# Kernel tuning notes

Hardware: AMD Instinct MI355X
Metric: run time of the kernel (lower is better)

## Reference

```python
import jax, jax.numpy as jnp
import numpy as np

B, S, D, H, L, MLP, WIN = 4, 1024, 256, 8, 2, 1024, 64
HD = D // H
NEG = -1e9  # emulates -inf additive mask; exp underflows to exact 0

_idx = jnp.arange(S)
BAND = jnp.where(jnp.abs(_idx[:, None] - _idx[None, :]) <= WIN, 0.0, NEG).astype(jnp.float32)


def setup_inputs() -> dict:
    key = jax.random.key(0)
    ks = iter(jax.random.split(key, 16))
    r = lambda shape, s=0.02: jax.random.normal(next(ks), shape, dtype=jnp.float32) * s
    return {
        "x": jax.random.normal(next(ks), (B, S, D), dtype=jnp.float32),
        "scale": jnp.ones((1,), jnp.float32) * (D ** -0.5),
        "Win_a": r((L, 3 * D, D)), "bin_a": jnp.zeros((L, 3 * D), jnp.float32),
        "Wout_a": r((L, D, D)), "bout_a": jnp.zeros((L, D), jnp.float32),
        "Win_e": r((L, 3 * D, D)), "bin_e": jnp.zeros((L, 3 * D), jnp.float32),
        "Wout_e": r((L, D, D)), "bout_e": jnp.zeros((L, D), jnp.float32),
        "ln1_g": jnp.ones((L, D), jnp.float32), "ln1_b": jnp.zeros((L, D), jnp.float32),
        "ln2_g": jnp.ones((L, D), jnp.float32), "ln2_b": jnp.zeros((L, D), jnp.float32),
        "W1": r((L, MLP, D)), "b1": jnp.zeros((L, MLP), jnp.float32),
        "W2": r((L, D, MLP)), "b2": jnp.zeros((L, D), jnp.float32),
        "lnf_g": jnp.ones((D,), jnp.float32), "lnf_b": jnp.zeros((D,), jnp.float32),
    }


def _layernorm(x, g, b, eps=1e-5):
    m = jnp.mean(x, axis=-1, keepdims=True)
    v = jnp.mean(jnp.square(x - m), axis=-1, keepdims=True)
    return (x - m) * jax.lax.rsqrt(v + eps) * g + b


def _mha(x, Win, bin_, Wout, bout, mask=None):
    # torch nn.MultiheadAttention (batch_first=True), dropout=0
    b, s, _ = x.shape
    qkv = x @ Win.T + bin_                       # (b, s, 3D)
    q, k, v = jnp.split(qkv, 3, axis=-1)
    split = lambda t: t.reshape(b, s, H, HD).transpose(0, 2, 1, 3)  # (b, H, s, HD)
    q, k, v = split(q), split(k), split(v)
    scores = jnp.einsum('bhqd,bhkd->bhqk', q, k) / np.float32(np.sqrt(HD))
    if mask is not None:
        scores = scores + mask
    attn = jax.nn.softmax(scores, axis=-1)
    out = jnp.einsum('bhqk,bhkd->bhqd', attn, v).transpose(0, 2, 1, 3).reshape(b, s, D)
    return out @ Wout.T + bout


def reference(x, scale, Win_a, bin_a, Wout_a, bout_a, Win_e, bin_e, Wout_e, bout_e,
              ln1_g, ln1_b, ln2_g, ln2_b, W1, b1, W2, b2, lnf_g, lnf_b):
    # ScaledSinusoidalPositionalEncoding returns arange(S)*scale, shape (S,1)
    pos = jnp.arange(S, dtype=jnp.float32) * scale[0]   # (S,)
    x = x + pos[:, None]                                 # broadcast (B,S,D)+(S,1)
    for l in range(L):
        xi = _mha(x, Win_a[l], bin_a[l], Wout_a[l], bout_a[l])
        x = _layernorm(x + xi, ln1_g[l], ln1_b[l])
        xe = _mha(x, Win_e[l], bin_e[l], Wout_e[l], bout_e[l], mask=BAND)
        attended = _layernorm(x + xe, ln2_g[l], ln2_b[l])
        h = jax.nn.gelu(attended @ W1[l].T + b1[l], approximate=False)
        x = attended + h @ W2[l].T + b2[l]
    return _layernorm(x, lnf_g, lnf_b)
```

## Files before the change

### kernel.cpp

```cpp
#include <hip/hip_runtime.h>
#include <math.h>

#define BB 4
#define SS 1024
#define DD 256
#define HH 8
#define HD 32
#define D3 768
#define MLP 1024
#define NTOK (BB * SS)
#define NSEG 4

typedef __attribute__((ext_vector_type(8))) short short8;
typedef __attribute__((ext_vector_type(4))) float f32x4;

__device__ __forceinline__ unsigned short f2bfu(float f) {
    union { float f; unsigned i; } u; u.f = f;
    unsigned r = u.i + 0x7fffu + ((u.i >> 16) & 1u);
    return (unsigned short)(r >> 16);
}
__device__ __forceinline__ float bfu2f(unsigned short h) {
    union { unsigned i; float f; } u; u.i = ((unsigned)h) << 16; return u.f;
}

#define W_TOT 2097152
#define WL0   196608
#define WBLK  (W_TOT / 256)
#define PBLK  (NTOK * DD / 256)
__global__ __launch_bounds__(256) void prep_kernel(
    const float* __restrict__ a0, const float* __restrict__ a1,
    const float* __restrict__ a2, const float* __restrict__ a3,
    const float* __restrict__ a4, const float* __restrict__ a5,
    unsigned short* __restrict__ out, unsigned short* __restrict__ out_lo,
    const float* __restrict__ x, const float* __restrict__ scale,
    float* __restrict__ xf, unsigned short* __restrict__ xh,
    unsigned short* __restrict__ xl)
{
    if (blockIdx.x < WBLK) {
        int i = blockIdx.x * 256 + threadIdx.x;
        const float* s; int off;
        if      (i <  393216) { s = a0; off = 0;       }
        else if (i <  524288) { s = a1; off = 393216;  }
        else if (i <  917504) { s = a2; off = 524288;  }
        else if (i < 1048576) { s = a3; off = 917504;  }
        else if (i < 1572864) { s = a4; off = 1048576; }
        else                  { s = a5; off = 1572864; }
        float v = s[i - off];
        unsigned short h = f2bfu(v);
        out[i] = h;
        if (i < WL0) out_lo[i] = f2bfu(v - bfu2f(h));
    } else {
        int i = (blockIdx.x - WBLK) * 256 + threadIdx.x;
        int s = (i >> 8) & (SS - 1);
        float v = x[i] + (float)s * scale[0];
        xf[i] = v;
        unsigned short h = f2bfu(v);
        xh[i] = h;
        xl[i] = f2bfu(v - bfu2f(h));
    }
}

__device__ __forceinline__ size_t vt_index(int row, int col512) {
    int b = row >> 10, s = row & (SS - 1);
    int h = col512 >> 5, d = col512 & (HD - 1);
    return (((size_t)b * HH + h) * HD + d) * SS + s;
}

#define LDP 40
__global__ __launch_bounds__(256) void gemm_mfma(
    const unsigned short* __restrict__ A, const unsigned short* __restrict__ W,
    const float* __restrict__ bias, const float* __restrict__ resid,
    float* __restrict__ outf, unsigned short* __restrict__ outb,
    unsigned short* __restrict__ vth,
    int M, int N, int K, int act)
{
    __shared__ __align__(16) unsigned short As[64 * LDP];
    __shared__ __align__(16) unsigned short Bs[128 * LDP];
    const int t = threadIdx.x;
    const int lane = t & 63, wave = t >> 6;
    const int wr = wave >> 1, wc = wave & 1;
    const int m0 = blockIdx.y * 64, n0 = blockIdx.x * 128;
    const int sr = t >> 2;
    const int sc = (t & 3) * 8;

    const unsigned short* Ag = A + (size_t)(m0 + sr) * K + sc;
    const unsigned short* Wg = W + (size_t)(n0 + sr) * K + sc;

    f32x4 acc[2][4];
    #pragma unroll
    for (int i = 0; i < 2; i++)
        #pragma unroll
        for (int j = 0; j < 4; j++)
            acc[i][j] = (f32x4){0.f, 0.f, 0.f, 0.f};

    const int lm = lane & 15, lk = (lane >> 4) * 8;

    uint4 a0 = *(const uint4*)(Ag);
    uint4 b0 = *(const uint4*)(Wg);
    uint4 b1 = *(const uint4*)(Wg + (size_t)64 * K);

    for (int k0 = 0; k0 < K; k0 += 32) {
        __syncthreads();
        *(uint4*)&As[sr * LDP + sc]        = a0;
        *(uint4*)&Bs[sr * LDP + sc]        = b0;
        *(uint4*)&Bs[(sr + 64) * LDP + sc] = b1;
        __syncthreads();
        if (k0 + 32 < K) {
            a0 = *(const uint4*)(Ag + k0 + 32);
            b0 = *(const uint4*)(Wg + k0 + 32);
            b1 = *(const uint4*)(Wg + (size_t)64 * K + k0 + 32);
        }

        short8 af[2], bf[4];
        #pragma unroll
        for (int i = 0; i < 2; i++)
            af[i] = *(const short8*)&As[(wr * 32 + i * 16 + lm) * LDP + lk];
        #pragma unroll
        for (int j = 0; j < 4; j++)
            bf[j] = *(const short8*)&Bs[(wc * 64 + j * 16 + lm) * LDP + lk];
        #pragma unroll
        for (int i = 0; i < 2; i++)
            #pragma unroll
            for (int j = 0; j < 4; j++)
                acc[i][j] = __builtin_amdgcn_mfma_f32_16x16x32_bf16(
                    af[i], bf[j], acc[i][j], 0, 0, 0);
    }

    const int lq = lane >> 4;
    #pragma unroll
    for (int j = 0; j < 4; j++) {
        int col = n0 + wc * 64 + j * 16 + lm;
        float bv = bias[col];
        #pragma unroll
        for (int i = 0; i < 2; i++) {
            #pragma unroll
            for (int r = 0; r < 4; r++) {
                int row = m0 + wr * 32 + i * 16 + lq * 4 + r;
                float v = acc[i][j][r] + bv;
                if (act) v = 0.5f * v * (1.0f + erff(v * 0.70710678118654752f));
                if (vth && col >= 2 * DD) {
                    vth[vt_index(row, col - 2 * DD)] = f2bfu(v);
                } else {
                    size_t idx = (size_t)row * N + col;
                    if (resid) v += resid[idx];
                    if (outf) outf[idx] = v;
                    if (outb) outb[idx] = f2bfu(v);
                }
            }
        }
    }
}

template<bool COMBINE, bool DOLN, int K>
__global__ __launch_bounds__(256) void gemm_ln(
    const unsigned short* __restrict__ A,
    const float* __restrict__ Of, const float2* __restrict__ Ml,
    const unsigned short* __restrict__ W, const float* __restrict__ bias,
    const float* __restrict__ resid,
    const float* __restrict__ g, const float* __restrict__ bt,
    float* __restrict__ outf, unsigned short* __restrict__ outb)
{
    constexpr int LDA = K + 8;
    constexpr int NS  = K / 32;
    __shared__ __align__(16) unsigned short As[16 * LDA];
    __shared__ float rsum[4][16];
    __shared__ float rsum2[4][16];
    const int t = threadIdx.x;
    const int lane = t & 63, wave = t >> 6;
    const int m0 = blockIdx.x * 16;
    const int lm = lane & 15, quad = lane >> 4;

    const unsigned short* Wp = W + (size_t)(wave * 64 + lm) * K + quad * 8;
    short8 bf[4][4];
    #pragma unroll
    for (int s = 0; s < 4; s++)
        #pragma unroll
        for (int j = 0; j < 4; j++)
            bf[s][j] = *(const short8*)(Wp + (size_t)(j * 16) * K + s * 32);

    if (COMBINE) {
        const int row = t >> 4, cg = t & 15;
        const int token = m0 + row;
        const int h = cg >> 1;
        float2 ml[NSEG];
        float M = -1e30f;
        #pragma unroll
        for (int s = 0; s < NSEG; s++) {
            ml[s] = Ml[((size_t)s * NTOK + token) * HH + h];
            M = fmaxf(M, ml[s].x);
        }
        float wgt[NSEG]; float denom = 0.f;
        #pragma unroll
        for (int s = 0; s < NSEG; s++) {
            wgt[s] = __expf(ml[s].x - M);
            denom += ml[s].y * wgt[s];
        }
        const float inv = 1.0f / denom;
        float a16[16];
        #pragma unroll
        for (int c = 0; c < 16; c++) a16[c] = 0.f;
        #pragma unroll
        for (int s = 0; s < NSEG; s++) {
            const float* p = Of + ((size_t)s * NTOK + token) * DD + cg * 16;
            #pragma unroll
            for (int c4 = 0; c4 < 4; c4++) {
                float4 x = *(const float4*)(p + c4 * 4);
                a16[c4 * 4 + 0] += x.x * wgt[s];
                a16[c4 * 4 + 1] += x.y * wgt[s];
                a16[c4 * 4 + 2] += x.z * wgt[s];
                a16[c4 * 4 + 3] += x.w * wgt[s];
            }
        }
        __align__(16) unsigned short ab[16];
        #pragma unroll
        for (int c = 0; c < 16; c++) ab[c] = f2bfu(a16[c] * inv);
        *(uint4*)&As[row * LDA + cg * 16]     = *(uint4*)&ab[0];
        *(uint4*)&As[row * LDA + cg * 16 + 8] = *(uint4*)&ab[8];
    } else {
        #pragma unroll
        for (int u = t; u < 16 * (K / 8); u += 256) {
            int row = u / (K / 8), cg = u % (K / 8);
            *(uint4*)&As[row * LDA + cg * 8] =
                *(const uint4*)(A + (size_t)(m0 + row) * K + cg * 8);
        }
    }
    __syncthreads();

    f32x4 acc[4];
    #pragma unroll
    for (int j = 0; j < 4; j++) acc[j] = (f32x4){0.f, 0.f, 0.f, 0.f};

    #pragma unroll
    for (int k = 0; k < NS; k++) {
        const int r4 = k & 3;
        short8 af = *(const short8*)&As[lm * LDA + k * 32 + quad * 8];
        #pragma unroll
        for (int j = 0; j < 4; j++)
            acc[j] = __builtin_amdgcn_mfma_f32_16x16x32_bf16(
                af, bf[r4][j], acc[j], 0, 0, 0);
        if (k + 4 < NS) {
            #pragma unroll
            for (int j = 0; j < 4; j++)
                bf[r4][j] = *(const short8*)(Wp + (size_t)(j * 16) * K
                                             + (k + 4) * 32);
        }
    }

    #pragma unroll
    for (int j = 0; j < 4; j++) {
        int col = wave * 64 + j * 16 + lm;
        float bv = bias[col];
        #pragma unroll
        for (int r = 0; r < 4; r++) {
            int row = m0 + quad * 4 + r;
            acc[j][r] += bv + resid[(size_t)row * DD + col];
        }
    }
    if (!DOLN) {
        #pragma unroll
        for (int j = 0; j < 4; j++) {
            int col = wave * 64 + j * 16 + lm;
            #pragma unroll
            for (int r = 0; r < 4; r++) {
                int row = m0 + quad * 4 + r;
                size_t idx = (size_t)row * DD + col;
                if (outf) outf[idx] = acc[j][r];
                if (outb) outb[idx] = f2bfu(acc[j][r]);
            }
        }
        return;
    }
    #pragma unroll
    for (int r = 0; r < 4; r++) {
        float s = 0.f;
        #pragma unroll
        for (int j = 0; j < 4; j++) s += acc[j][r];
        s += __shfl_xor(s, 1, 64); s += __shfl_xor(s, 2, 64);
        s += __shfl_xor(s, 4, 64); s += __shfl_xor(s, 8, 64);
        if (lm == 0) rsum[wave][quad * 4 + r] = s;
    }
    __syncthreads();
    float mean_[4];
    #pragma unroll
    for (int r = 0; r < 4; r++) {
        int ri = quad * 4 + r;
        mean_[r] = (rsum[0][ri] + rsum[1][ri] + rsum[2][ri] + rsum[3][ri])
                 * (1.0f / 256.0f);
    }
    #pragma unroll
    for (int r = 0; r < 4; r++) {
        float s2 = 0.f;
        #pragma unroll
        for (int j = 0; j < 4; j++) {
            float d = acc[j][r] - mean_[r];
            s2 += d * d;
        }
        s2 += __shfl_xor(s2, 1, 64); s2 += __shfl_xor(s2, 2, 64);
        s2 += __shfl_xor(s2, 4, 64); s2 += __shfl_xor(s2, 8, 64);
        if (lm == 0) rsum2[wave][quad * 4 + r] = s2;
    }
    __syncthreads();
    float rstd[4];
    #pragma unroll
    for (int r = 0; r < 4; r++) {
        int ri = quad * 4 + r;
        rstd[r] = rsqrtf((rsum2[0][ri] + rsum2[1][ri] + rsum2[2][ri] + rsum2[3][ri])
                         * (1.0f / 256.0f) + 1e-5f);
    }
    #pragma unroll
    for (int j = 0; j < 4; j++) {
        int col = wave * 64 + j * 16 + lm;
        float gv = g[col], bv2 = bt[col];
        #pragma unroll
        for (int r = 0; r < 4; r++) {
            int row = m0 + quad * 4 + r;
            float ov = (acc[j][r] - mean_[r]) * rstd[r] * gv + bv2;
            size_t idx = (size_t)row * DD + col;
            if (outf) outf[idx] = ov;
            if (outb) outb[idx] = f2bfu(ov);
        }
    }
}

__global__ __launch_bounds__(256) void gemm_mfma_split(
    const unsigned short* __restrict__ Ah, const unsigned short* __restrict__ Al,
    const unsigned short* __restrict__ Wh, const unsigned short* __restrict__ Wl,
    const float* __restrict__ bias,
    unsigned short* __restrict__ outh, unsigned short* __restrict__ outl,
    unsigned short* __restrict__ vth,
    int M, int N, int K)
{
    __shared__ __align__(16) unsigned short Ash[64 * LDP];
    __shared__ __align__(16) unsigned short Asl[64 * LDP];
    __shared__ __align__(16) unsigned short Bsh[128 * LDP];
    __shared__ __align__(16) unsigned short Bsl[128 * LDP];
    const int t = threadIdx.x;
    const int lane = t & 63, wave = t >> 6;
    const int wr = wave >> 1, wc = wave & 1;
    const int m0 = blockIdx.y * 64, n0 = blockIdx.x * 128;
    const int sr = t >> 2;
    const int sc = (t & 3) * 8;

    const size_t oA = (size_t)(m0 + sr) * K + sc;
    const size_t oW = (size_t)(n0 + sr) * K + sc;

    f32x4 acc[2][4];
    #pragma unroll
    for (int i = 0; i < 2; i++)
        #pragma unroll
        for (int j = 0; j < 4; j++)
            acc[i][j] = (f32x4){0.f, 0.f, 0.f, 0.f};

    const int lm = lane & 15, lk = (lane >> 4) * 8;

    uint4 ah0 = *(const uint4*)(Ah + oA);
    uint4 al0 = *(const uint4*)(Al + oA);
    uint4 bh0 = *(const uint4*)(Wh + oW);
    uint4 bh1 = *(const uint4*)(Wh + oW + (size_t)64 * K);
    uint4 bl0 = *(const uint4*)(Wl + oW);
    uint4 bl1 = *(const uint4*)(Wl + oW + (size_t)64 * K);

    for (int k0 = 0; k0 < K; k0 += 32) {
        __syncthreads();
        *(uint4*)&Ash[sr * LDP + sc]        = ah0;
        *(uint4*)&Asl[sr * LDP + sc]        = al0;
        *(uint4*)&Bsh[sr * LDP + sc]        = bh0;
        *(uint4*)&Bsh[(sr + 64) * LDP + sc] = bh1;
        *(uint4*)&Bsl[sr * LDP + sc]        = bl0;
        *(uint4*)&Bsl[(sr + 64) * LDP + sc] = bl1;
        __syncthreads();
        if (k0 + 32 < K) {
            ah0 = *(const uint4*)(Ah + oA + k0 + 32);
            al0 = *(const uint4*)(Al + oA + k0 + 32);
            bh0 = *(const uint4*)(Wh + oW + k0 + 32);
            bh1 = *(const uint4*)(Wh + oW + (size_t)64 * K + k0 + 32);
            bl0 = *(const uint4*)(Wl + oW + k0 + 32);
            bl1 = *(const uint4*)(Wl + oW + (size_t)64 * K + k0 + 32);
        }

        short8 afh[2], afl[2], bfh[4], bfl[4];
        #pragma unroll
        for (int i = 0; i < 2; i++) {
            afh[i] = *(const short8*)&Ash[(wr * 32 + i * 16 + lm) * LDP + lk];
            afl[i] = *(const short8*)&Asl[(wr * 32 + i * 16 + lm) * LDP + lk];
        }
        #pragma unroll
        for (int j = 0; j < 4; j++) {
            bfh[j] = *(const short8*)&Bsh[(wc * 64 + j * 16 + lm) * LDP + lk];
            bfl[j] = *(const short8*)&Bsl[(wc * 64 + j * 16 + lm) * LDP + lk];
        }
        #pragma unroll
        for (int i = 0; i < 2; i++)
            #pragma unroll
            for (int j = 0; j < 4; j++) {
                acc[i][j] = __builtin_amdgcn_mfma_f32_16x16x32_bf16(
                    afl[i], bfh[j], acc[i][j], 0, 0, 0);
                acc[i][j] = __builtin_amdgcn_mfma_f32_16x16x32_bf16(
                    afh[i], bfl[j], acc[i][j], 0, 0, 0);
                acc[i][j] = __builtin_amdgcn_mfma_f32_16x16x32_bf16(
                    afh[i], bfh[j], acc[i][j], 0, 0, 0);
            }
    }

    const int lq = lane >> 4;
    #pragma unroll
    for (int j = 0; j < 4; j++) {
        int col = n0 + wc * 64 + j * 16 + lm;
        float bv = bias[col];
        #pragma unroll
        for (int i = 0; i < 2; i++) {
            #pragma unroll
            for (int r = 0; r < 4; r++) {
                int row = m0 + wr * 32 + i * 16 + lq * 4 + r;
                float v = acc[i][j][r] + bv;
                unsigned short h = f2bfu(v);
                if (col >= 2 * DD) {
                    vth[vt_index(row, col - 2 * DD)] = h;
                } else {
                    size_t idx = (size_t)row * N + col;
                    outh[idx] = h;
                    outl[idx] = f2bfu(v - bfu2f(h));
                }
            }
        }
    }
}

__global__ __launch_bounds__(256) void attn_split(
    const unsigned short* __restrict__ qkvh,
    const unsigned short* __restrict__ qkvl,
    const unsigned short* __restrict__ vth,
    float* __restrict__ Of, float2* __restrict__ Ml)
{
    __shared__ __align__(16) unsigned short Ks [64 * 40];
    __shared__ __align__(16) unsigned short Vt [32 * 72];
    __shared__ __align__(16) unsigned short Ps [64 * 72];
    __shared__ __align__(16) unsigned short Ksl[64 * 40];

    const int t = threadIdx.x;
    const int wave = t >> 6, lane = t & 63;
    const int lm = lane & 15, quad = lane >> 4;
    const int i0 = blockIdx.x * 64, h = blockIdx.y;
    const int z = blockIdx.z;
    const int b = z >> 2, seg = z & (NSEG - 1);
    const int sr = t >> 2, sc8 = (t & 3) * 8;
    const int vd = t >> 3, vs8 = (t & 7) * 8;

    const size_t qoff = ((size_t)(b * SS) + i0 + 16 * wave + lm) * D3 + h * HD + quad * 8;
    short8 qh = *(const short8*)(qkvh + qoff);
    short8 ql = *(const short8*)(qkvl + qoff);

    const unsigned short* Kg  = qkvh + (size_t)(b * SS) * D3 + DD + h * HD;
    const unsigned short* Klg = qkvl + (size_t)(b * SS) * D3 + DD + h * HD;
    const unsigned short* Vg  = vth + ((size_t)b * HH + h) * HD * SS;

    float m[4], l[4];
    f32x4 o[2];
    #pragma unroll
    for (int r = 0; r < 4; r++) { m[r] = -1e30f; l[r] = 0.f; }
    o[0] = (f32x4){0.f, 0.f, 0.f, 0.f};
    o[1] = (f32x4){0.f, 0.f, 0.f, 0.f};

    const int per = (SS / 64) / NSEG;
    const int s0 = seg * per, s1 = s0 + per - 1;
    const float scl = 0.17677669529663688f;

    short8 kreg  = *(const short8*)(Kg  + (size_t)(s0 * 64 + sr) * D3 + sc8);
    short8 kregl = *(const short8*)(Klg + (size_t)(s0 * 64 + sr) * D3 + sc8);
    short8 vreg  = *(const short8*)(Vg  + (size_t)vd * SS + s0 * 64 + vs8);

    for (int kt = s0; kt <= s1; kt++) {
        const int k0 = kt * 64;
        __syncthreads();
        *(short8*)&Ks [sr * 40 + sc8] = kreg;
        *(short8*)&Ksl[sr * 40 + sc8] = kregl;
        *(short8*)&Vt [vd * 72 + vs8] = vreg;
        __syncthreads();
        if (kt < s1) {
            kreg  = *(const short8*)(Kg  + (size_t)(k0 + 64 + sr) * D3 + sc8);
            kregl = *(const short8*)(Klg + (size_t)(k0 + 64 + sr) * D3 + sc8);
            vreg  = *(const short8*)(Vg  + (size_t)vd * SS + k0 + 64 + vs8);
        }

        f32x4 s[4];
        #pragma unroll
        for (int cb = 0; cb < 4; cb++) {
            short8 kf  = *(const short8*)&Ks [(16 * cb + lm) * 40 + quad * 8];
            short8 kfl = *(const short8*)&Ksl[(16 * cb + lm) * 40 + quad * 8];
            f32x4 a = (f32x4){0.f, 0.f, 0.f, 0.f};
            a = __builtin_amdgcn_mfma_f32_16x16x32_bf16(ql, kf,  a, 0, 0, 0);
            a = __builtin_amdgcn_mfma_f32_16x16x32_bf16(qh, kfl, a, 0, 0, 0);
            a = __builtin_amdgcn_mfma_f32_16x16x32_bf16(qh, kf,  a, 0, 0, 0);
            s[cb] = a;
        }

        #pragma unroll
        for (int r = 0; r < 4; r++) {
            float s0r = s[0][r] * scl, s1r = s[1][r] * scl;
            float s2r = s[2][r] * scl, s3r = s[3][r] * scl;
            float tm = fmaxf(fmaxf(s0r, s1r), fmaxf(s2r, s3r));
            tm = fmaxf(tm, __shfl_xor(tm, 1, 64));
            tm = fmaxf(tm, __shfl_xor(tm, 2, 64));
            tm = fmaxf(tm, __shfl_xor(tm, 4, 64));
            tm = fmaxf(tm, __shfl_xor(tm, 8, 64));
            float mn = fmaxf(m[r], tm);
            float alpha = __expf(m[r] - mn);
            float p0 = __expf(s0r - mn), p1 = __expf(s1r - mn);
            float p2 = __expf(s2r - mn), p3 = __expf(s3r - mn);
            float ps = p0 + p1 + p2 + p3;
            ps += __shfl_xor(ps, 1, 64);
            ps += __shfl_xor(ps, 2, 64);
            ps += __shfl_xor(ps, 4, 64);
            ps += __shfl_xor(ps, 8, 64);
            l[r] = l[r] * alpha + ps;
            o[0][r] *= alpha;
            o[1][r] *= alpha;
            m[r] = mn;
            const int pr = (16 * wave + quad * 4 + r) * 72 + lm;
            Ps[pr +  0] = f2bfu(p0);
            Ps[pr + 16] = f2bfu(p1);
            Ps[pr + 32] = f2bfu(p2);
            Ps[pr + 48] = f2bfu(p3);
        }

        #pragma unroll
        for (int kc = 0; kc < 2; kc++) {
            short8 pf = *(const short8*)&Ps[(16 * wave + lm) * 72 + 32 * kc + quad * 8];
            #pragma unroll
            for (int nh = 0; nh < 2; nh++) {
                short8 vf = *(const short8*)&Vt[(16 * nh + lm) * 72 + 32 * kc + quad * 8];
                o[nh] = __builtin_amdgcn_mfma_f32_16x16x32_bf16(pf, vf, o[nh], 0, 0, 0);
            }
        }
    }

    #pragma unroll
    for (int r = 0; r < 4; r++) {
        int row = i0 + 16 * wave + quad * 4 + r;
        size_t base = ((size_t)seg * NTOK + b * SS + row) * DD + h * HD + lm;
        Of[base]      = o[0][r];
        Of[base + 16] = o[1][r];
        if (lm == 0)
            Ml[((size_t)seg * NTOK + b * SS + row) * HH + h] =
                make_float2(m[r], l[r]);
    }
}

__global__ __launch_bounds__(256) void attn_fixed(
    const unsigned short* __restrict__ qkvh,
    const unsigned short* __restrict__ vth,
    unsigned short* __restrict__ outb,
    float* __restrict__ Of, float2* __restrict__ Ml,
    int win, int nseg)
{
    __shared__ __align__(16) unsigned short Ks[64 * 40];
    __shared__ __align__(16) unsigned short Vt[32 * 72];
    __shared__ __align__(16) unsigned short Ps[64 * 72];

    const int t = threadIdx.x;
    const int wave = t >> 6, lane = t & 63;
    const int lm = lane & 15, quad = lane >> 4;
    const int i0 = blockIdx.x * 64, h = blockIdx.y;
    const int z = blockIdx.z;
    const int b = z / nseg, seg = z - b * nseg;
    const int sr = t >> 2, sc8 = (t & 3) * 8;
    const int vd = t >> 3, vs8 = (t & 7) * 8;

    const size_t qoff = ((size_t)(b * SS) + i0 + 16 * wave + lm) * D3 + h * HD + quad * 8;
    short8 qh = *(const short8*)(qkvh + qoff);

    const unsigned short* Kg = qkvh + (size_t)(b * SS) * D3 + DD + h * HD;
    const unsigned short* Vg = vth + ((size_t)b * HH + h) * HD * SS;

    float l[4] = {0.f, 0.f, 0.f, 0.f};
    f32x4 o[2];
    o[0] = (f32x4){0.f, 0.f, 0.f, 0.f};
    o[1] = (f32x4){0.f, 0.f, 0.f, 0.f};

    int t0 = 0, t1 = SS / 64 - 1;
    const bool masked = (win < SS);
    if (masked) {
        t0 = (i0 - win) >> 6;        if (t0 < 0) t0 = 0;
        t1 = (i0 + 63 + win) >> 6;   if (t1 > SS / 64 - 1) t1 = SS / 64 - 1;
    }
    const int per = (t1 - t0 + nseg) / nseg;
    const int s0 = t0 + seg * per;
    const int s1 = (s0 + per - 1 < t1) ? (s0 + per - 1) : t1;
    const float scl = 0.17677669529663688f;
    const float M0 = 32.0f;

    short8 kreg = *(const short8*)(Kg + (size_t)(s0 * 64 + sr) * D3 + sc8);
    short8 vreg = *(const short8*)(Vg + (size_t)vd * SS + s0 * 64 + vs8);

    for (int kt = s0; kt <= s1; kt++) {
        const int k0 = kt * 64;
        __syncthreads();
        *(short8*)&Ks[sr * 40 + sc8] = kreg;
        *(short8*)&Vt[vd * 72 + vs8] = vreg;
        __syncthreads();
        if (kt < s1) {
            kreg = *(const short8*)(Kg + (size_t)(k0 + 64 + sr) * D3 + sc8);
            vreg = *(const short8*)(Vg + (size_t)vd * SS + k0 + 64 + vs8);
        }

        f32x4 s[4];
        #pragma unroll
        for (int cb = 0; cb < 4; cb++) {
            short8 kf = *(const short8*)&Ks[(16 * cb + lm) * 40 + quad * 8];
            f32x4 a = (f32x4){0.f, 0.f, 0.f, 0.f};
            a = __builtin_amdgcn_mfma_f32_16x16x32_bf16(qh, kf, a, 0, 0, 0);
            s[cb] = a;
        }

        #pragma unroll
        for (int r = 0; r < 4; r++) {
            float p[4];
            #pragma unroll
            for (int cb = 0; cb < 4; cb++) {
                float v = s[cb][r] * scl;
                if (masked) {
                    int di = (i0 + 16 * wave + quad * 4 + r) - (k0 + 16 * cb + lm);
                    if (di > win || di < -win) v = -1e30f;
                }
                p[cb] = __expf(v - M0);
            }
            l[r] += p[0] + p[1] + p[2] + p[3];
            const int pr = (16 * wave + quad * 4 + r) * 72 + lm;
            Ps[pr +  0] = f2bfu(p[0]);
            Ps[pr + 16] = f2bfu(p[1]);
            Ps[pr + 32] = f2bfu(p[2]);
            Ps[pr + 48] = f2bfu(p[3]);
        }

        #pragma unroll
        for (int kc = 0; kc < 2; kc++) {
            short8 pf = *(const short8*)&Ps[(16 * wave + lm) * 72 + 32 * kc + quad * 8];
            #pragma unroll
            for (int nh = 0; nh < 2; nh++) {
                short8 vf = *(const short8*)&Vt[(16 * nh + lm) * 72 + 32 * kc + quad * 8];
                o[nh] = __builtin_amdgcn_mfma_f32_16x16x32_bf16(pf, vf, o[nh], 0, 0, 0);
            }
        }
    }

    #pragma unroll
    for (int r = 0; r < 4; r++) {
        l[r] += __shfl_xor(l[r], 1, 64);
        l[r] += __shfl_xor(l[r], 2, 64);
        l[r] += __shfl_xor(l[r], 4, 64);
        l[r] += __shfl_xor(l[r], 8, 64);
    }

    if (nseg == 1) {
        #pragma unroll
        for (int r = 0; r < 4; r++) {
            float invl = 1.0f / l[r];
            size_t base = ((size_t)(b * SS) + i0 + 16 * wave + quad * 4 + r) * DD + h * HD + lm;
            outb[base]      = f2bfu(o[0][r] * invl);
            outb[base + 16] = f2bfu(o[1][r] * invl);
        }
    } else {
        #pragma unroll
        for (int r = 0; r < 4; r++) {
            int row = i0 + 16 * wave + quad * 4 + r;
            size_t base = ((size_t)seg * NTOK + b * SS + row) * DD + h * HD + lm;
            Of[base]      = o[0][r];
            Of[base + 16] = o[1][r];
            if (lm == 0)
                Ml[((size_t)seg * NTOK + b * SS + row) * HH + h] =
                    make_float2(M0, l[r]);
        }
    }
}

extern "C" void kernel_launch(void* const* d_in, const int* in_sizes, int n_in,
                              void* d_out, int out_size, void* d_ws, size_t ws_size,
                              hipStream_t stream)
{
    const float* xin   = (const float*)d_in[0];
    const float* scale = (const float*)d_in[1];
    const float* Win_a = (const float*)d_in[2];
    const float* bin_a = (const float*)d_in[3];
    const float* Wout_a= (const float*)d_in[4];
    const float* bout_a= (const float*)d_in[5];
    const float* Win_e = (const float*)d_in[6];
    const float* bin_e = (const float*)d_in[7];
    const float* Wout_e= (const float*)d_in[8];
    const float* bout_e= (const float*)d_in[9];
    const float* ln1_g = (const float*)d_in[10];
    const float* ln1_b = (const float*)d_in[11];
    const float* ln2_g = (const float*)d_in[12];
    const float* ln2_b = (const float*)d_in[13];
    const float* W1    = (const float*)d_in[14];
    const float* b1    = (const float*)d_in[15];
    const float* W2    = (const float*)d_in[16];
    const float* b2    = (const float*)d_in[17];
    const float* lnf_g = (const float*)d_in[18];
    const float* lnf_b = (const float*)d_in[19];

    char* ws = (char*)d_ws;
    float* X    = (float*)ws;                     ws += (size_t)NTOK * DD * 4;
    float* X2   = (float*)ws;                     ws += (size_t)NTOK * DD * 4;
    unsigned short* Xb   = (unsigned short*)ws;   ws += (size_t)NTOK * DD * 2;
    unsigned short* Xlb  = (unsigned short*)ws;   ws += (size_t)NTOK * DD * 2;
    unsigned short* X2b  = (unsigned short*)ws;   ws += (size_t)NTOK * DD * 2;
    unsigned short* ATb  = (unsigned short*)ws;   ws += (size_t)NTOK * DD * 2;
    unsigned short* QKVb = (unsigned short*)ws;   ws += (size_t)NTOK * D3 * 2;
    unsigned short* QKVl = (unsigned short*)ws;   ws += (size_t)NTOK * D3 * 2;
    unsigned short* VTh  = (unsigned short*)ws;   ws += (size_t)NTOK * DD * 2;
    unsigned short* HMLb = (unsigned short*)ws;   ws += (size_t)NTOK * MLP * 2;
    unsigned short* Wb   = (unsigned short*)ws;   ws += (size_t)W_TOT * 2;
    unsigned short* Wl0  = (unsigned short*)ws;   ws += (size_t)WL0 * 2;
    float2* Ml           = (float2*)ws;           ws += (size_t)NSEG * NTOK * HH * 8;
    float* Of            = (float*)ws;            ws += (size_t)NSEG * NTOK * DD * 4;

    unsigned short* WinA_b  = Wb + 0;
    unsigned short* WoutA_b = Wb + 393216;
    unsigned short* WinE_b  = Wb + 524288;
    unsigned short* WoutE_b = Wb + 917504;
    unsigned short* W1_b    = Wb + 1048576;
    unsigned short* W2_b    = Wb + 1572864;

    prep_kernel<<<WBLK + PBLK, 256, 0, stream>>>(
        Win_a, Wout_a, Win_e, Wout_e, W1, W2, Wb, Wl0,
        xin, scale, X, Xb, Xlb);

    float* cur = X;            float* oth = X2;
    unsigned short* curb = Xb; unsigned short* othb = X2b;

    for (int l = 0; l < 2; l++) {
        if (l == 0) {
            gemm_mfma_split<<<dim3(D3 / 128, NTOK / 64), 256, 0, stream>>>(
                Xb, Xlb, WinA_b, Wl0, bin_a, QKVb, QKVl, VTh, NTOK, D3, DD);
            attn_split<<<dim3(SS / 64, HH, BB * NSEG), 256, 0, stream>>>(
                QKVb, QKVl, VTh, Of, Ml);
        } else {
            gemm_mfma<<<dim3(D3 / 128, NTOK / 64), 256, 0, stream>>>(
                curb, WinA_b + (size_t)l * D3 * DD, bin_a + (size_t)l * D3,
                nullptr, nullptr, QKVb, VTh, NTOK, D3, DD, 0);
            attn_fixed<<<dim3(SS / 64, HH, BB * NSEG), 256, 0, stream>>>(
                QKVb, VTh, nullptr, Of, Ml, 1 << 28, NSEG);
        }
        gemm_ln<true, true, DD><<<NTOK / 16, 256, 0, stream>>>(
            nullptr, Of, Ml, WoutA_b + (size_t)l * DD * DD,
            bout_a + (size_t)l * DD, cur,
            ln1_g + l * DD, ln1_b + l * DD, oth, othb);

        gemm_mfma<<<dim3(D3 / 128, NTOK / 64), 256, 0, stream>>>(
            othb, WinE_b + (size_t)l * D3 * DD, bin_e + (size_t)l * D3,
            nullptr, nullptr, QKVb, VTh, NTOK, D3, DD, 0);
        attn_fixed<<<dim3(SS / 64, HH, BB), 256, 0, stream>>>(
            QKVb, VTh, ATb, nullptr, nullptr, 64, 1);
        gemm_ln<false, true, DD><<<NTOK / 16, 256, 0, stream>>>(
            ATb, nullptr, nullptr, WoutE_b + (size_t)l * DD * DD,
            bout_e + (size_t)l * DD, oth,
            ln2_g + l * DD, ln2_b + l * DD, cur, curb);

        gemm_mfma<<<dim3(MLP / 128, NTOK / 64), 256, 0, stream>>>(
            curb, W1_b + (size_t)l * MLP * DD, b1 + (size_t)l * MLP,
            nullptr, nullptr, HMLb, nullptr, NTOK, MLP, DD, 1);
        if (l == 0) {
            gemm_ln<false, false, MLP><<<NTOK / 16, 256, 0, stream>>>(
                HMLb, nullptr, nullptr, W2_b + (size_t)l * DD * MLP,
                b2 + (size_t)l * DD, cur,
                nullptr, nullptr, oth, othb);
            float* tf = cur; cur = oth; oth = tf;
            unsigned short* tb = curb; curb = othb; othb = tb;
        } else {
            gemm_ln<false, true, MLP><<<NTOK / 16, 256, 0, stream>>>(
                HMLb, nullptr, nullptr, W2_b + (size_t)l * DD * MLP,
                b2 + (size_t)l * DD, cur,
                lnf_g, lnf_b, (float*)d_out, nullptr);
        }
    }
}
```

Measured before the change: 317.8 us.

## Stage full-K A tile in LDS and stream weights directly into registers

The QKV and MLP-up GEMMs (K=256) now load the whole 64xK activation tile into LDS once, with a single barrier, instead of looping over 32-wide K chunks with two barriers each. The weight fragments are read straight from global memory into registers through a small rotating prefetch buffer (4 stages, or 2 for the hi/lo split kernel), so the B tile no longer goes through shared memory. This removes per-step synchronisation and LDS traffic. In exchange it uses more registers and LDS (about 33KB per block, 66KB for the split kernel), which may lower occupancy, and each wave re-reads weights from global or L2.

Result: slower. 354.7 us (+11.6%).

```diff
diff --git a/kernel.cpp b/kernel.cpp
--- a/kernel.cpp
+++ b/kernel.cpp
@@ -66,25 +66,38 @@
     return (((size_t)b * HH + h) * HD + d) * SS + s;
 }
 
-#define LDP 40
+template<int KK>
 __global__ __launch_bounds__(256) void gemm_mfma(
     const unsigned short* __restrict__ A, const unsigned short* __restrict__ W,
     const float* __restrict__ bias, const float* __restrict__ resid,
     float* __restrict__ outf, unsigned short* __restrict__ outb,
     unsigned short* __restrict__ vth,
-    int M, int N, int K, int act)
+    int N, int act)
 {
-    __shared__ __align__(16) unsigned short As[64 * LDP];
-    __shared__ __align__(16) unsigned short Bs[128 * LDP];
+    constexpr int LDA = KK + 8;
+    constexpr int NS  = KK / 32;
+    __shared__ __align__(16) unsigned short As[64 * LDA];
     const int t = threadIdx.x;
     const int lane = t & 63, wave = t >> 6;
     const int wr = wave >> 1, wc = wave & 1;
     const int m0 = blockIdx.y * 64, n0 = blockIdx.x * 128;
-    const int sr = t >> 2;
-    const int sc = (t & 3) * 8;
-
-    const unsigned short* Ag = A + (size_t)(m0 + sr) * K + sc;
-    const unsigned short* Wg = W + (size_t)(n0 + sr) * K + sc;
+    const int lm = lane & 15, quad = lane >> 4;
+
+    const unsigned short* Wp = W + (size_t)(n0 + wc * 64 + lm) * KK + quad * 8;
+    short8 bf[4][4];
+    #pragma unroll
+    for (int s = 0; s < 4; s++)
+        #pragma unroll
+        for (int j = 0; j < 4; j++)
+            bf[s][j] = *(const short8*)(Wp + (size_t)(j * 16) * KK + s * 32);
+
+    #pragma unroll
+    for (int i = 0; i < (64 * KK) / (256 * 8); i++) {
+        int idx = (t + i * 256) * 8;
+        int row = idx / KK, c = idx % KK;
+        *(uint4*)&As[row * LDA + c] = *(const uint4*)(A + (size_t)(m0 + row) * KK + c);
+    }
+    __syncthreads();
 
     f32x4 acc[2][4];
     #pragma unroll
@@ -93,40 +106,27 @@
         for (int j = 0; j < 4; j++)
             acc[i][j] = (f32x4){0.f, 0.f, 0.f, 0.f};
 
-    const int lm = lane & 15, lk = (lane >> 4) * 8;
-
-    uint4 a0 = *(const uint4*)(Ag);
-    uint4 b0 = *(const uint4*)(Wg);
-    uint4 b1 = *(const uint4*)(Wg + (size_t)64 * K);
-
-    for (int k0 = 0; k0 < K; k0 += 32) {
-        __syncthreads();
-        *(uint4*)&As[sr * LDP + sc]        = a0;
-        *(uint4*)&Bs[sr * LDP + sc]        = b0;
-        *(uint4*)&Bs[(sr + 64) * LDP + sc] = b1;
-        __syncthreads();
-        if (k0 + 32 < K) {
-            a0 = *(const uint4*)(Ag + k0 + 32);
-            b0 = *(const uint4*)(Wg + k0 + 32);
-            b1 = *(const uint4*)(Wg + (size_t)64 * K + k0 + 32);
-        }
-
-        short8 af[2], bf[4];
+    #pragma unroll
+    for (int k = 0; k < NS; k++) {
+        const int r4 = k & 3;
+        short8 af[2];
         #pragma unroll
         for (int i = 0; i < 2; i++)
-            af[i] = *(const short8*)&As[(wr * 32 + i * 16 + lm) * LDP + lk];
-        #pragma unroll
-        for (int j = 0; j < 4; j++)
-            bf[j] = *(const short8*)&Bs[(wc * 64 + j * 16 + lm) * LDP + lk];
+            af[i] = *(const short8*)&As[(wr * 32 + i * 16 + lm) * LDA + k * 32 + quad * 8];
         #pragma unroll
         for (int i = 0; i < 2; i++)
             #pragma unroll
             for (int j = 0; j < 4; j++)
                 acc[i][j] = __builtin_amdgcn_mfma_f32_16x16x32_bf16(
-                    af[i], bf[j], acc[i][j], 0, 0, 0);
-    }
-
-    const int lq = lane >> 4;
+                    af[i], bf[r4][j], acc[i][j], 0, 0, 0);
+        if (k + 4 < NS) {
+            #pragma unroll
+            for (int j = 0; j < 4; j++)
+                bf[r4][j] = *(const short8*)(Wp + (size_t)(j * 16) * KK + (k + 4) * 32);
+        }
+    }
+
+    const int lq = quad;
     #pragma unroll
     for (int j = 0; j < 4; j++) {
         int col = n0 + wc * 64 + j * 16 + lm;
@@ -328,21 +328,38 @@
     const float* __restrict__ bias,
     unsigned short* __restrict__ outh, unsigned short* __restrict__ outl,
     unsigned short* __restrict__ vth,
-    int M, int N, int K)
+    int N)
 {
-    __shared__ __align__(16) unsigned short Ash[64 * LDP];
-    __shared__ __align__(16) unsigned short Asl[64 * LDP];
-    __shared__ __align__(16) unsigned short Bsh[128 * LDP];
-    __shared__ __align__(16) unsigned short Bsl[128 * LDP];
+    constexpr int KK  = DD;
+    constexpr int LDA = KK + 8;
+    constexpr int NS  = KK / 32;
+    __shared__ __align__(16) unsigned short Ash[64 * LDA];
+    __shared__ __align__(16) unsigned short Asl[64 * LDA];
     const int t = threadIdx.x;
     const int lane = t & 63, wave = t >> 6;
     const int wr = wave >> 1, wc = wave & 1;
     const int m0 = blockIdx.y * 64, n0 = blockIdx.x * 128;
-    const int sr = t >> 2;
-    const int sc = (t & 3) * 8;
-
-    const size_t oA = (size_t)(m0 + sr) * K + sc;
-    const size_t oW = (size_t)(n0 + sr) * K + sc;
+    const int lm = lane & 15, quad = lane >> 4;
+
+    const unsigned short* Wph = Wh + (size_t)(n0 + wc * 64 + lm) * KK + quad * 8;
+    const unsigned short* Wpl = Wl + (size_t)(n0 + wc * 64 + lm) * KK + quad * 8;
+    short8 bfh[2][4], bfl[2][4];
+    #pragma unroll
+    for (int s = 0; s < 2; s++)
+        #pragma unroll
+        for (int j = 0; j < 4; j++) {
+            bfh[s][j] = *(const short8*)(Wph + (size_t)(j * 16) * KK + s * 32);
+            bfl[s][j] = *(const short8*)(Wpl + (size_t)(j * 16) * KK + s * 32);
+        }
+
+    #pragma unroll
+    for (int i = 0; i < (64 * KK) / (256 * 8); i++) {
+        int idx = (t + i * 256) * 8;
+        int row = idx / KK, c = idx % KK;
+        *(uint4*)&Ash[row * LDA + c] = *(const uint4*)(Ah + (size_t)(m0 + row) * KK + c);
+        *(uint4*)&Asl[row * LDA + c] = *(const uint4*)(Al + (size_t)(m0 + row) * KK + c);
+    }
+    __syncthreads();
 
     f32x4 acc[2][4];
     #pragma unroll
@@ -351,58 +368,36 @@
         for (int j = 0; j < 4; j++)
             acc[i][j] = (f32x4){0.f, 0.f, 0.f, 0.f};
 
-    const int lm = lane & 15, lk = (lane >> 4) * 8;
-
-    uint4 ah0 = *(const uint4*)(Ah + oA);
-    uint4 al0 = *(const uint4*)(Al + oA);
-    uint4 bh0 = *(const uint4*)(Wh + oW);
-    uint4 bh1 = *(const uint4*)(Wh + oW + (size_t)64 * K);
-    uint4 bl0 = *(const uint4*)(Wl + oW);
-    uint4 bl1 = *(const uint4*)(Wl + oW + (size_t)64 * K);
-
-    for (int k0 = 0; k0 < K; k0 += 32) {
-        __syncthreads();
-        *(uint4*)&Ash[sr * LDP + sc]        = ah0;
-        *(uint4*)&Asl[sr * LDP + sc]        = al0;
-        *(uint4*)&Bsh[sr * LDP + sc]        = bh0;
-        *(uint4*)&Bsh[(sr + 64) * LDP + sc] = bh1;
-        *(uint4*)&Bsl[sr * LDP + sc]        = bl0;
-        *(uint4*)&Bsl[(sr + 64) * LDP + sc] = bl1;
-        __syncthreads();
-        if (k0 + 32 < K) {
-            ah0 = *(const uint4*)(Ah + oA + k0 + 32);
-            al0 = *(const uint4*)(Al + oA + k0 + 32);
-            bh0 = *(const uint4*)(Wh + oW + k0 + 32);
-            bh1 = *(const uint4*)(Wh + oW + (size_t)64 * K + k0 + 32);
-            bl0 = *(const uint4*)(Wl + oW + k0 + 32);
-            bl1 = *(const uint4*)(Wl + oW + (size_t)64 * K + k0 + 32);
-        }
-
-        short8 afh[2], afl[2], bfh[4], bfl[4];
+    #pragma unroll
+    for (int k = 0; k < NS; k++) {
+        const int r2 = k & 1;
+        short8 afh[2], afl[2];
         #pragma unroll
         for (int i = 0; i < 2; i++) {
-            afh[i] = *(const short8*)&Ash[(wr * 32 + i * 16 + lm) * LDP + lk];
-            afl[i] = *(const short8*)&Asl[(wr * 32 + i * 16 + lm) * LDP + lk];
-        }
-        #pragma unroll
-        for (int j = 0; j < 4; j++) {
-            bfh[j] = *(const short8*)&Bsh[(wc * 64 + j * 16 + lm) * LDP + lk];
-            bfl[j] = *(const short8*)&Bsl[(wc * 64 + j * 16 + lm) * LDP + lk];
+            afh[i] = *(const short8*)&Ash[(wr * 32 + i * 16 + lm) * LDA + k * 32 + quad * 8];
+            afl[i] = *(const short8*)&Asl[(wr * 32 + i * 16 + lm) * LDA + k * 32 + quad * 8];
         }
         #pragma unroll
         for (int i = 0; i < 2; i++)
             #pragma unroll
             for (int j = 0; j < 4; j++) {
                 acc[i][j] = __builtin_amdgcn_mfma_f32_16x16x32_bf16(
-                    afl[i], bfh[j], acc[i][j], 0, 0, 0);
+                    afl[i], bfh[r2][j], acc[i][j], 0, 0, 0);
                 acc[i][j] = __builtin_amdgcn_mfma_f32_16x16x32_bf16(
-                    afh[i], bfl[j], acc[i][j], 0, 0, 0);
+                    afh[i], bfl[r2][j], acc[i][j], 0, 0, 0);
                 acc[i][j] = __builtin_amdgcn_mfma_f32_16x16x32_bf16(
-                    afh[i], bfh[j], acc[i][j], 0, 0, 0);
-            }
-    }
-
-    const int lq = lane >> 4;
+                    afh[i], bfh[r2][j], acc[i][j], 0, 0, 0);
+            }
+        if (k + 2 < NS) {
+            #pragma unroll
+            for (int j = 0; j < 4; j++) {
+                bfh[r2][j] = *(const short8*)(Wph + (size_t)(j * 16) * KK + (k + 2) * 32);
+                bfl[r2][j] = *(const short8*)(Wpl + (size_t)(j * 16) * KK + (k + 2) * 32);
+            }
+        }
+    }
+
+    const int lq = quad;
     #pragma unroll
     for (int j = 0; j < 4; j++) {
         int col = n0 + wc * 64 + j * 16 + lm;
@@ -731,13 +726,13 @@
     for (int l = 0; l < 2; l++) {
         if (l == 0) {
             gemm_mfma_split<<<dim3(D3 / 128, NTOK / 64), 256, 0, stream>>>(
-                Xb, Xlb, WinA_b, Wl0, bin_a, QKVb, QKVl, VTh, NTOK, D3, DD);
+                Xb, Xlb, WinA_b, Wl0, bin_a, QKVb, QKVl, VTh, D3);
             attn_split<<<dim3(SS / 64, HH, BB * NSEG), 256, 0, stream>>>(
                 QKVb, QKVl, VTh, Of, Ml);
         } else {
-            gemm_mfma<<<dim3(D3 / 128, NTOK / 64), 256, 0, stream>>>(
+            gemm_mfma<DD><<<dim3(D3 / 128, NTOK / 64), 256, 0, stream>>>(
                 curb, WinA_b + (size_t)l * D3 * DD, bin_a + (size_t)l * D3,
-                nullptr, nullptr, QKVb, VTh, NTOK, D3, DD, 0);
+                nullptr, nullptr, QKVb, VTh, D3, 0);
             attn_fixed<<<dim3(SS / 64, HH, BB * NSEG), 256, 0, stream>>>(
                 QKVb, VTh, nullptr, Of, Ml, 1 << 28, NSEG);
         }
@@ -746,9 +741,9 @@
             bout_a + (size_t)l * DD, cur,
             ln1_g + l * DD, ln1_b + l * DD, oth, othb);
 
-        gemm_mfma<<<dim3(D3 / 128, NTOK / 64), 256, 0, stream>>>(
+        gemm_mfma<DD><<<dim3(D3 / 128, NTOK / 64), 256, 0, stream>>>(
             othb, WinE_b + (size_t)l * D3 * DD, bin_e + (size_t)l * D3,
-            nullptr, nullptr, QKVb, VTh, NTOK, D3, DD, 0);
+            nullptr, nullptr, QKVb, VTh, D3, 0);
         attn_fixed<<<dim3(SS / 64, HH, BB), 256, 0, stream>>>(
             QKVb, VTh, ATb, nullptr, nullptr, 64, 1);
         gemm_ln<false, true, DD><<<NTOK / 16, 256, 0, stream>>>(
@@ -756,9 +751,9 @@
             bout_e + (size_t)l * DD, oth,
             ln2_g + l * DD, ln2_b + l * DD, cur, curb);
 
-        gemm_mfma<<<dim3(MLP / 128, NTOK / 64), 256, 0, stream>>>(
+        gemm_mfma<DD><<<dim3(MLP / 128, NTOK / 64), 256, 0, stream>>>(
             curb, W1_b + (size_t)l * MLP * DD, b1 + (size_t)l * MLP,
-            nullptr, nullptr, HMLb, nullptr, NTOK, MLP, DD, 1);
+            nullptr, nullptr, HMLb, nullptr, MLP, 1);
         if (l == 0) {
             gemm_ln<false, false, MLP><<<NTOK / 16, 256, 0, stream>>>(
                 HMLb, nullptr, nullptr, W2_b + (size_t)l * DD * MLP,
```
